# Kernel optimization log

Measured on AMD Instinct MI355X. Metric: run time of the kernel, lower is better.

## Reference

```python
import jax, jax.numpy as jnp
import numpy as np

F = 128
NRBF = 20
CUTOFF = 5.0
L = 3
NZ = 100
F2 = F // 2
N = 10000
E = 256000
NMOL = 100
EPS = 1e-8


def setup_inputs() -> dict:
    key = jax.random.key(0)
    ks = jax.random.split(key, 20)
    xyz = jax.random.uniform(ks[0], (N, 3), jnp.float32) * 10.0
    z = jax.random.randint(ks[1], (N,), 0, NZ)
    nbrs = jax.random.randint(ks[2], (E, 2), 0, N)
    # avoid self-edges (would give zero distance in the sinc RBF)
    nbrs = nbrs.at[:, 1].set(jnp.where(nbrs[:, 1] == nbrs[:, 0], (nbrs[:, 1] + 1) % N, nbrs[:, 1]))
    mol_idx = jnp.sort(jax.random.randint(ks[3], (N,), 0, NMOL))

    def p(k, shape, scale=0.05):
        return jax.random.normal(k, shape, jnp.float32) * scale

    return dict(
        xyz=xyz, z=z, nbrs=nbrs, mol_idx=mol_idx,
        emb=p(ks[4], (NZ, F), 1.0),
        msg_W1=p(ks[5], (L, F, F)), msg_b1=jnp.zeros((L, F), jnp.float32),
        msg_W2=p(ks[6], (L, F, 3 * F)), msg_b2=jnp.zeros((L, 3 * F), jnp.float32),
        dist_W=p(ks[7], (L, NRBF, 3 * F)), dist_b=jnp.zeros((L, 3 * F), jnp.float32),
        upd_U=p(ks[8], (L, F, F)), upd_V=p(ks[9], (L, F, F)),
        upd_W1=p(ks[10], (L, 2 * F, F)), upd_b1=jnp.zeros((L, F), jnp.float32),
        upd_W2=p(ks[11], (L, F, 3 * F)), upd_b2=jnp.zeros((L, 3 * F), jnp.float32),
        read_W1=p(ks[12], (F, F2)), read_b1=jnp.zeros((F2,), jnp.float32),
        read_W2=p(ks[13], (F2, 1)), read_b2=jnp.zeros((1,), jnp.float32),
    )


def _painn(xyz, emb, msg_W1, msg_b1, msg_W2, msg_b2, dist_W, dist_b,
           upd_U, upd_V, upd_W1, upd_b1, upd_W2, upd_b2,
           read_W1, read_b1, read_W2, read_b2, z, nbrs, mol_idx):
    idx_i = nbrs[:, 0]
    idx_j = nbrs[:, 1]
    r_ij = xyz[idx_j] - xyz[idx_i]                       # [E,3]
    d = jnp.sqrt(jnp.sum(r_ij * r_ij, -1) + EPS)          # [E]
    unit = r_ij / d[:, None]
    # sinc radial basis + cosine cutoff envelope
    nvec = jnp.arange(1, NRBF + 1, dtype=xyz.dtype)
    rbf = jnp.sin(nvec[None, :] * jnp.pi * d[:, None] / CUTOFF) / d[:, None]   # [E,NRBF]
    fcut = 0.5 * (jnp.cos(jnp.pi * d / CUTOFF) + 1.0) * (d < CUTOFF)           # [E]

    s_i = emb[z]                                          # [N,F]
    v_i = jnp.zeros((xyz.shape[0], F, 3), xyz.dtype)      # [N,F,3]

    for l in range(L):
        # message block: invariant filter on nodes, gather to edges
        phi = (jax.nn.silu(s_i @ msg_W1[l] + msg_b1[l]) @ msg_W2[l] + msg_b2[l])[idx_j]  # [E,3F]
        w_s = (rbf @ dist_W[l] + dist_b[l]) * fcut[:, None]                               # [E,3F]
        inv = (phi * w_s).reshape(-1, 3, F)
        ds_edge = inv[:, 0]                                                               # [E,F]
        dv_edge = inv[:, 1][:, :, None] * v_i[idx_j] + inv[:, 2][:, :, None] * unit[:, None, :]  # [E,F,3]
        s_i = s_i + jax.ops.segment_sum(ds_edge, idx_i, num_segments=s_i.shape[0])
        v_i = v_i + jax.ops.segment_sum(dv_edge, idx_i, num_segments=s_i.shape[0])

        # update block: channel-mixing of vectors + gated scalar/vector residuals
        u_v = jnp.einsum('nfv,fg->ngv', v_i, upd_U[l])
        v_v = jnp.einsum('nfv,fg->ngv', v_i, upd_V[l])
        vnorm = jnp.sqrt(jnp.sum(v_v * v_v, -1) + EPS)                                    # [N,F]
        a = (jax.nn.silu(jnp.concatenate([s_i, vnorm], -1) @ upd_W1[l] + upd_b1[l])
             @ upd_W2[l] + upd_b2[l]).reshape(-1, 3, F)
        dv = u_v * a[:, 0][:, :, None]
        ds = a[:, 1] * jnp.sum(u_v * v_v, -1) + a[:, 2]
        s_i = s_i + ds
        v_i = v_i + dv

    atom_e = jax.nn.silu(s_i @ read_W1 + read_b1) @ read_W2 + read_b2                     # [N,1]
    energy = jax.ops.segment_sum(atom_e[:, 0], mol_idx, num_segments=NMOL)                # [NMOL]
    return energy


def reference(xyz, z, nbrs, mol_idx, emb, msg_W1, msg_b1, msg_W2, msg_b2,
              dist_W, dist_b, upd_U, upd_V, upd_W1, upd_b1, upd_W2, upd_b2,
              read_W1, read_b1, read_W2, read_b2):
    return _painn(xyz, emb, msg_W1, msg_b1, msg_W2, msg_b2, dist_W, dist_b,
                  upd_U, upd_V, upd_W1, upd_b1, upd_W2, upd_b2,
                  read_W1, read_b1, read_W2, read_b2, z, nbrs, mol_idx)
```

## Files before the change

kernel.cpp:

```cpp
#include <hip/hip_runtime.h>
#include <hip/hip_bf16.h>
#include <math.h>

#define NA 10000
#define NE 256000
#define FDIM 128
#define F3 384
#define NRBF 20
#define NLAYERS 3
#define NMOLS 100
#define CAP 96
#define WROW 388
#define PACK_BLOCKS 2288
#define CUTOFF_F 5.0f
#define EPS_F 1e-8f
#define PI_F 3.14159265358979323846f

typedef __attribute__((ext_vector_type(8))) short bf16x8;
typedef __attribute__((ext_vector_type(4))) float f32x4;

struct pv6 { unsigned int u0, u1, u2; };

__device__ __forceinline__ float silu_f(float x) { return x / (1.0f + __expf(-x)); }

__device__ __forceinline__ unsigned short f2bf(float x) {
  unsigned u = __float_as_uint(x);
  return (unsigned short)((u + 0x7FFFu + ((u >> 16) & 1u)) >> 16);
}
__device__ __forceinline__ float bf2f(unsigned short u) {
  return __uint_as_float(((unsigned)u) << 16);
}
__device__ __forceinline__ float lo_f(unsigned int u) { return bf2f((unsigned short)(u & 0xFFFFu)); }
__device__ __forceinline__ float hi_f(unsigned int u) { return bf2f((unsigned short)(u >> 16)); }

__device__ __forceinline__ void bar_lds() {
  asm volatile("s_waitcnt lgkmcnt(0)" ::: "memory");
  __builtin_amdgcn_s_barrier();
}

__device__ __forceinline__ void pack_one(const float* __restrict__ src,
                                         unsigned short* __restrict__ dst,
                                         int loc, int per, int N) {
  int lay = loc / per;
  int kn = loc - lay * per;
  int k = kn / N, n = kn - k * N;
  int kb = k >> 5, q = (k >> 3) & 3, j = k & 7, nt = n >> 4, c = n & 15;
  int NT = N >> 4;
  dst[(size_t)lay * per + (((kb * NT + nt) * 64 + (q * 16 + c)) * 8 + j)] = f2bf(src[loc]);
}

__device__ __forceinline__ void pack_dw(const float* __restrict__ dW,
                                        const float* __restrict__ db,
                                        unsigned short* __restrict__ dst, int loc) {
  int lay = loc / 12288;
  int kn = loc - lay * 12288;
  int k = kn / 384, n = kn - k * 384;
  float val = 0.0f;
  if (k < NRBF) val = dW[lay * NRBF * 384 + k * 384 + n];
  else if (k == NRBF) val = db[lay * 384 + n];
  int q = (k >> 3) & 3, j = k & 7, nt = n >> 4, c = n & 15;
  dst[(size_t)lay * 12288 + ((nt * 64 + (q * 16 + c)) * 8 + j)] = f2bf(val);
}

__global__ __launch_bounds__(256) void prep_kernel(
    const float* __restrict__ msgW1, const float* __restrict__ msgW2,
    const float* __restrict__ updU, const float* __restrict__ updV,
    const float* __restrict__ updW1, const float* __restrict__ updW2,
    const float* __restrict__ rW1, const float* __restrict__ distW,
    const float* __restrict__ distb, unsigned short* __restrict__ dst,
    const float* __restrict__ xyz, const int* __restrict__ nbrs,
    float* __restrict__ unitv, unsigned short* __restrict__ rbf_bf,
    float* __restrict__ fcut,
    int* __restrict__ deg, int* __restrict__ slot_e, int* __restrict__ slot_j) {
  int b = blockIdx.x;
  if (b < PACK_BLOCKS) {
    int t = b * 256 + threadIdx.x;
    if (t < 49152) pack_one(msgW1, dst, t, 16384, 128);
    else if (t < 196608) pack_one(msgW2, dst + 49152, t - 49152, 49152, 384);
    else if (t < 245760) pack_one(updU, dst + 196608, t - 196608, 16384, 128);
    else if (t < 294912) pack_one(updV, dst + 245760, t - 245760, 16384, 128);
    else if (t < 393216) pack_one(updW1, dst + 294912, t - 294912, 32768, 128);
    else if (t < 540672) pack_one(updW2, dst + 393216, t - 393216, 49152, 384);
    else if (t < 548864) pack_one(rW1, dst + 540672, t - 540672, 8192, 64);
    else if (t < 585728) pack_dw(distW, distb, dst + 548864, t - 548864);
    return;
  }
  int e = (b - PACK_BLOCKS) * 256 + threadIdx.x;
  if (e >= NE) return;
  int i = nbrs[2 * e + 0], j = nbrs[2 * e + 1];
  float rx = xyz[3 * j + 0] - xyz[3 * i + 0];
  float ry = xyz[3 * j + 1] - xyz[3 * i + 1];
  float rz = xyz[3 * j + 2] - xyz[3 * i + 2];
  float d = sqrtf(rx * rx + ry * ry + rz * rz + EPS_F);
  if (d >= CUTOFF_F) return;
  float invd = 1.0f / d;
  float fc = 0.5f * (__cosf(PI_F * d / CUTOFF_F) + 1.0f);
  unitv[3 * e + 0] = rx * invd;
  unitv[3 * e + 1] = ry * invd;
  unitv[3 * e + 2] = rz * invd;
  fcut[e] = fc;
  float base = PI_F * d / CUTOFF_F;
  float sc = invd * fc;
#pragma unroll
  for (int k = 0; k < NRBF; k++)
    rbf_bf[(size_t)e * NRBF + k] = f2bf(__sinf((float)(k + 1) * base) * sc);
  int pos = atomicAdd(&deg[i], 1);
  if (pos < CAP) {
    slot_e[i * CAP + pos] = e;
    slot_j[i * CAP + pos] = j;
  }
}

__global__ __launch_bounds__(256) void msg0_mfma_kernel(
    const float* __restrict__ emb, const int* __restrict__ z, float* __restrict__ s_out,
    const unsigned short* __restrict__ pW1, const float* __restrict__ b1,
    const unsigned short* __restrict__ pW2, const float* __restrict__ b2,
    pv6* __restrict__ cmb) {
  __shared__ bf16x8 sA[4 * 64];
  __shared__ bf16x8 hA[4 * 64];
  int a0 = blockIdx.x * 16;
  int t = threadIdx.x;
  int lane = t & 63, w = t >> 6;
  {
    int kb = t >> 6, l = t & 63;
    int m = l & 15, q = l >> 4;
    int zi = z[a0 + m];
    const float* sp = emb + (size_t)zi * FDIM + kb * 32 + q * 8;
    float* so = s_out + (size_t)(a0 + m) * FDIM + kb * 32 + q * 8;
    bf16x8 c;
#pragma unroll
    for (int j = 0; j < 8; j++) {
      float v = sp[j];
      so[j] = v;
      c[j] = (short)f2bf(v);
    }
    sA[kb * 64 + l] = c;
  }
  __syncthreads();
  f32x4 accH[2];
#pragma unroll
  for (int t2 = 0; t2 < 2; t2++)
#pragma unroll
    for (int r = 0; r < 4; r++) accH[t2][r] = 0.0f;
  const bf16x8* W1f = (const bf16x8*)pW1;
#pragma unroll
  for (int kb = 0; kb < 4; kb++) {
    bf16x8 a = sA[kb * 64 + lane];
#pragma unroll
    for (int t2 = 0; t2 < 2; t2++) {
      bf16x8 b = W1f[(kb * 8 + 2 * w + t2) * 64 + lane];
      accH[t2] = __builtin_amdgcn_mfma_f32_16x16x32_bf16(a, b, accH[t2], 0, 0, 0);
    }
  }
  short* hs = (short*)hA;
#pragma unroll
  for (int t2 = 0; t2 < 2; t2++) {
    int n = w * 32 + t2 * 16 + (lane & 15);
    int kb = n >> 5, q = (n >> 3) & 3, j = n & 7;
    float bias = b1[n];
#pragma unroll
    for (int r = 0; r < 4; r++) {
      int m = (lane >> 4) * 4 + r;
      hs[(kb * 64 + q * 16 + m) * 8 + j] = (short)f2bf(silu_f(accH[t2][r] + bias));
    }
  }
  __syncthreads();
  f32x4 accP[3][2];
#pragma unroll
  for (int c3 = 0; c3 < 3; c3++)
#pragma unroll
    for (int t2 = 0; t2 < 2; t2++)
#pragma unroll
      for (int r = 0; r < 4; r++) accP[c3][t2][r] = 0.0f;
  const bf16x8* W2f = (const bf16x8*)pW2;
#pragma unroll
  for (int kb = 0; kb < 4; kb++) {
    bf16x8 a = hA[kb * 64 + lane];
#pragma unroll
    for (int c3 = 0; c3 < 3; c3++)
#pragma unroll
      for (int t2 = 0; t2 < 2; t2++) {
        bf16x8 b = W2f[(kb * 24 + c3 * 8 + 2 * w + t2) * 64 + lane];
        accP[c3][t2] = __builtin_amdgcn_mfma_f32_16x16x32_bf16(a, b, accP[c3][t2], 0, 0, 0);
      }
  }
#pragma unroll
  for (int t2 = 0; t2 < 2; t2++) {
    int g = (2 * w + t2) * 16 + (lane & 15);
    float bb0 = b2[g], bb1 = b2[FDIM + g], bb2 = b2[2 * FDIM + g];
#pragma unroll
    for (int r = 0; r < 4; r++) {
      int m = (lane >> 4) * 4 + r;
      unsigned p0 = f2bf(accP[0][t2][r] + bb0);
      unsigned p1 = f2bf(accP[1][t2][r] + bb1);
      unsigned p2 = f2bf(accP[2][t2][r] + bb2);
      pv6 rec;
      rec.u0 = p0 | (p1 << 16);
      rec.u1 = p2;
      rec.u2 = 0;
      cmb[(size_t)(a0 + m) * FDIM + g] = rec;
    }
  }
}

__device__ __forceinline__ void afrag_load(const unsigned short* __restrict__ rbf_bf,
                                           const float* __restrict__ fcut,
                                           const int* l_e_all, int cnt, int c0,
                                           int m16, int q4,
                                           unsigned short apf[8], float* afc) {
#pragma unroll
  for (int j = 0; j < 8; j++) apf[j] = 0;
  *afc = 0.0f;
  int p = c0 + m16;
  if (p < cnt && q4 < 3) {
    int e = l_e_all[p];
    const unsigned short* rb = rbf_bf + (size_t)e * NRBF;
    if (q4 < 2) {
#pragma unroll
      for (int j = 0; j < 8; j++) apf[j] = rb[q4 * 8 + j];
    } else {
#pragma unroll
      for (int j = 0; j < 4; j++) apf[j] = rb[16 + j];
      *afc = fcut[e];
    }
  }
}

__device__ __forceinline__ void pref4(const pv6* __restrict__ cmb, const int* l_j,
                                      int cnt, int p0, int f, pv6 R[4]) {
#pragma unroll
  for (int u = 0; u < 4; u++) {
    if (p0 + u < cnt) R[u] = cmb[(size_t)l_j[p0 + u] * FDIM + f];
  }
}

__device__ __forceinline__ void proc4(const pv6 R[4], int pp, int ccnt, int f,
                                      const unsigned short (*w_lds)[WROW],
                                      const float (*l_u)[3],
                                      float& acc_s, float& av0, float& av1, float& av2) {
#pragma unroll
  for (int u = 0; u < 4; u++) {
    if (pp + u < ccnt) {
      float p0 = lo_f(R[u].u0), p1 = hi_f(R[u].u0), p2 = lo_f(R[u].u1);
      float v0 = hi_f(R[u].u1), v1 = lo_f(R[u].u2), v2 = hi_f(R[u].u2);
      float w0 = bf2f(w_lds[pp + u][f]), w1 = bf2f(w_lds[pp + u][FDIM + f]),
            w2 = bf2f(w_lds[pp + u][2 * FDIM + f]);
      acc_s += p0 * w0;
      float i1 = p1 * w1, i2 = p2 * w2;
      av0 += i1 * v0 + i2 * l_u[pp + u][0];
      av1 += i1 * v1 + i2 * l_u[pp + u][1];
      av2 += i1 * v2 + i2 * l_u[pp + u][2];
    }
  }
}

__global__ __launch_bounds__(128) void edge_kernel(
    const pv6* __restrict__ cmb, unsigned short* __restrict__ v_lin,
    float* __restrict__ s, const unsigned short* __restrict__ pDW,
    const int* __restrict__ deg, const int* __restrict__ slot_e,
    const int* __restrict__ slot_j, const unsigned short* __restrict__ rbf_bf,
    const float* __restrict__ fcut, const float* __restrict__ unitv) {
  __shared__ unsigned short w_lds[16][WROW];
  __shared__ float l_u[16][3];
  __shared__ int l_e_all[CAP];
  __shared__ int l_j_all[CAP];
  int i = blockIdx.x;
  int t = threadIdx.x;
  int f = t;
  int lane = t & 63, w = t >> 6;
  int cnt = deg[i];
  if (cnt > CAP) cnt = CAP;
  int base = i * CAP;
  if (t < cnt) {
    l_e_all[t] = slot_e[base + t];
    l_j_all[t] = slot_j[base + t];
  }
  __syncthreads();
  float acc_s = 0.f, av0 = 0.f, av1 = 0.f, av2 = 0.f;
  const bf16x8* Bf = (const bf16x8*)pDW;
  int m16 = lane & 15, q4 = lane >> 4;
  unsigned short apf[8];
  float afc = 0.0f;
  pv6 Ra[4], Rb[4];
  if (cnt > 0) {
    afrag_load(rbf_bf, fcut, l_e_all, cnt, 0, m16, q4, apf, &afc);
    pref4(cmb, l_j_all, cnt, 0, f, Ra);
  }
  for (int c0 = 0; c0 < cnt; c0 += 16) {
    int ccnt = cnt - c0;
    if (ccnt > 16) ccnt = 16;
    bar_lds();
    if (t >= 64 && t < 80) {
      int idx = t - 64, p = c0 + idx;
      if (p < cnt) {
        int e = l_e_all[p];
        l_u[idx][0] = unitv[3 * e + 0];
        l_u[idx][1] = unitv[3 * e + 1];
        l_u[idx][2] = unitv[3 * e + 2];
      }
    }
    bf16x8 a;
#pragma unroll
    for (int j = 0; j < 8; j++) a[j] = (short)apf[j];
    if (q4 == 2) a[4] = (short)f2bf(afc);
    {
      int n0 = lane & 15, mm0 = (lane >> 4) * 4;
#pragma unroll
      for (int tt = 0; tt < 12; tt++) {
        int nt = 12 * w + tt;
        f32x4 acc;
#pragma unroll
        for (int r = 0; r < 4; r++) acc[r] = 0.0f;
        acc = __builtin_amdgcn_mfma_f32_16x16x32_bf16(a, Bf[nt * 64 + lane], acc, 0, 0, 0);
        int n = nt * 16 + n0;
#pragma unroll
        for (int r = 0; r < 4; r++) w_lds[mm0 + r][n] = f2bf(acc[r]);
      }
    }
    if (c0 + 16 < cnt) afrag_load(rbf_bf, fcut, l_e_all, cnt, c0 + 16, m16, q4, apf, &afc);
    bar_lds();
    pref4(cmb, l_j_all, cnt, c0 + 4, f, Rb);
    proc4(Ra, 0, ccnt, f, w_lds, l_u, acc_s, av0, av1, av2);
    pref4(cmb, l_j_all, cnt, c0 + 8, f, Ra);
    proc4(Rb, 4, ccnt, f, w_lds, l_u, acc_s, av0, av1, av2);
    pref4(cmb, l_j_all, cnt, c0 + 12, f, Rb);
    proc4(Ra, 8, ccnt, f, w_lds, l_u, acc_s, av0, av1, av2);
    pref4(cmb, l_j_all, cnt, c0 + 16, f, Ra);
    proc4(Rb, 12, ccnt, f, w_lds, l_u, acc_s, av0, av1, av2);
  }
  {
    pv6 RI = cmb[(size_t)i * FDIM + f];
    av0 += hi_f(RI.u1);
    av1 += lo_f(RI.u2);
    av2 += hi_f(RI.u2);
  }
  unsigned short* vlo = v_lin + (size_t)i * F3;
  vlo[f] = f2bf(av0);
  vlo[FDIM + f] = f2bf(av1);
  vlo[2 * FDIM + f] = f2bf(av2);
  s[(size_t)i * FDIM + f] += acc_s;
}

__global__ __launch_bounds__(256) void upd_fused_kernel(
    float* __restrict__ s, const unsigned short* __restrict__ v_lin,
    pv6* __restrict__ cmb,
    const unsigned short* __restrict__ pU, const unsigned short* __restrict__ pV,
    const unsigned short* __restrict__ pW1, const float* __restrict__ b1,
    const unsigned short* __restrict__ pW2, const float* __restrict__ b2,
    int mode,
    const unsigned short* __restrict__ pMW1, const float* __restrict__ mb1,
    const unsigned short* __restrict__ pMW2, const float* __restrict__ mb2,
    const unsigned short* __restrict__ pRW1, const float* __restrict__ rb1,
    const float* __restrict__ rW2, const float* __restrict__ rb2,
    float* __restrict__ atom_e) {
  __shared__ bf16x8 vAf[3 * 4 * 64];
  __shared__ bf16x8 catA[8 * 64];
  __shared__ bf16x8 hA[4 * 64];
  __shared__ float red[4][16];
  int a0 = blockIdx.x * 16;
  int t = threadIdx.x;
  int lane = t & 63, w = t >> 6;
  {
    int l = t & 63, kb = (t >> 6) & 3;
    int m = l & 15, q = l >> 4;
#pragma unroll
    for (int rt = 0; rt < 3; rt++) {
      vAf[(rt * 4 + kb) * 64 + l] =
          *(const bf16x8*)(v_lin + (size_t)(a0 + m) * F3 + rt * FDIM + kb * 32 + q * 8);
    }
    const float* sp = s + (size_t)(a0 + m) * FDIM + kb * 32 + q * 8;
    bf16x8 c;
#pragma unroll
    for (int j = 0; j < 8; j++) c[j] = (short)f2bf(sp[j]);
    catA[kb * 64 + l] = c;
  }
  __syncthreads();
  f32x4 accU[3][2], accV[3][2];
#pragma unroll
  for (int rt = 0; rt < 3; rt++)
#pragma unroll
    for (int t2 = 0; t2 < 2; t2++)
#pragma unroll
      for (int r = 0; r < 4; r++) { accU[rt][t2][r] = 0.0f; accV[rt][t2][r] = 0.0f; }
  const bf16x8* Uf = (const bf16x8*)pU;
  const bf16x8* Vf = (const bf16x8*)pV;
#pragma unroll
  for (int kb = 0; kb < 4; kb++) {
    bf16x8 bu[2], bv[2];
#pragma unroll
    for (int t2 = 0; t2 < 2; t2++) {
      bu[t2] = Uf[(kb * 8 + 2 * w + t2) * 64 + lane];
      bv[t2] = Vf[(kb * 8 + 2 * w + t2) * 64 + lane];
    }
#pragma unroll
    for (int rt = 0; rt < 3; rt++) {
      bf16x8 a = vAf[(rt * 4 + kb) * 64 + lane];
#pragma unroll
      for (int t2 = 0; t2 < 2; t2++) {
        accU[rt][t2] = __builtin_amdgcn_mfma_f32_16x16x32_bf16(a, bu[t2], accU[rt][t2], 0, 0, 0);
        accV[rt][t2] = __builtin_amdgcn_mfma_f32_16x16x32_bf16(a, bv[t2], accV[rt][t2], 0, 0, 0);
      }
    }
  }
  short* cs = (short*)catA;
#pragma unroll
  for (int t2 = 0; t2 < 2; t2++) {
    int g = w * 32 + t2 * 16 + (lane & 15);
    int k = 128 + g;
    int kb = k >> 5, q = (k >> 3) & 3, j = k & 7;
#pragma unroll
    for (int r = 0; r < 4; r++) {
      int m = (lane >> 4) * 4 + r;
      float x0 = accV[0][t2][r], x1 = accV[1][t2][r], x2 = accV[2][t2][r];
      cs[(kb * 64 + q * 16 + m) * 8 + j] = (short)f2bf(sqrtf(x0 * x0 + x1 * x1 + x2 * x2 + EPS_F));
    }
  }
  __syncthreads();
  f32x4 accH[2];
#pragma unroll
  for (int t2 = 0; t2 < 2; t2++)
#pragma unroll
    for (int r = 0; r < 4; r++) accH[t2][r] = 0.0f;
  const bf16x8* W1f = (const bf16x8*)pW1;
#pragma unroll
  for (int kb = 0; kb < 8; kb++) {
    bf16x8 a = catA[kb * 64 + lane];
#pragma unroll
    for (int t2 = 0; t2 < 2; t2++) {
      bf16x8 b = W1f[(kb * 8 + 2 * w + t2) * 64 + lane];
      accH[t2] = __builtin_amdgcn_mfma_f32_16x16x32_bf16(a, b, accH[t2], 0, 0, 0);
    }
  }
  short* hs = (short*)hA;
#pragma unroll
  for (int t2 = 0; t2 < 2; t2++) {
    int n = w * 32 + t2 * 16 + (lane & 15);
    int kb = n >> 5, q = (n >> 3) & 3, j = n & 7;
    float bias = b1[n];
#pragma unroll
    for (int r = 0; r < 4; r++) {
      int m = (lane >> 4) * 4 + r;
      hs[(kb * 64 + q * 16 + m) * 8 + j] = (short)f2bf(silu_f(accH[t2][r] + bias));
    }
  }
  __syncthreads();
  f32x4 accA[3][2];
#pragma unroll
  for (int c3 = 0; c3 < 3; c3++)
#pragma unroll
    for (int t2 = 0; t2 < 2; t2++)
#pragma unroll
      for (int r = 0; r < 4; r++) accA[c3][t2][r] = 0.0f;
  const bf16x8* W2f = (const bf16x8*)pW2;
#pragma unroll
  for (int kb = 0; kb < 4; kb++) {
    bf16x8 a = hA[kb * 64 + lane];
#pragma unroll
    for (int c3 = 0; c3 < 3; c3++)
#pragma unroll
      for (int t2 = 0; t2 < 2; t2++) {
        bf16x8 b = W2f[(kb * 24 + c3 * 8 + 2 * w + t2) * 64 + lane];
        accA[c3][t2] = __builtin_amdgcn_mfma_f32_16x16x32_bf16(a, b, accA[c3][t2], 0, 0, 0);
      }
  }
  const short* vls = (const short*)vAf;
  unsigned short v0keep[2][4];
#pragma unroll
  for (int t2 = 0; t2 < 2; t2++) {
    int g = w * 32 + t2 * 16 + (lane & 15);
    float bb0 = b2[g], bb1 = b2[FDIM + g], bb2 = b2[2 * FDIM + g];
    int kb = g >> 5, q = (g >> 3) & 3, j = g & 7;
#pragma unroll
    for (int r = 0; r < 4; r++) {
      int m = (lane >> 4) * 4 + r;
      int n = a0 + m;
      float a0v = accA[0][t2][r] + bb0;
      float a1v = accA[1][t2][r] + bb1;
      float a2v = accA[2][t2][r] + bb2;
      float dot = accU[0][t2][r] * accV[0][t2][r] + accU[1][t2][r] * accV[1][t2][r] +
                  accU[2][t2][r] * accV[2][t2][r];
      float s_new = s[(size_t)n * FDIM + g] + a1v * dot + a2v;
      if (mode == 0) {
        s[(size_t)n * FDIM + g] = s_new;
        float nv[3];
#pragma unroll
        for (int c = 0; c < 3; c++) {
          float vold = bf2f((unsigned short)vls[(((c * 4 + kb) * 64) + (q * 16 + m)) * 8 + j]);
          nv[c] = vold + a0v * accU[c][t2][r];
        }
        v0keep[t2][r] = f2bf(nv[0]);
        cmb[(size_t)n * FDIM + g].u2 = (unsigned)f2bf(nv[1]) | ((unsigned)f2bf(nv[2]) << 16);
      }
      cs[(kb * 64 + q * 16 + m) * 8 + j] = (short)f2bf(s_new);
    }
  }
  __syncthreads();
  if (mode == 0) {
    f32x4 accH2[2];
#pragma unroll
    for (int t2 = 0; t2 < 2; t2++)
#pragma unroll
      for (int r = 0; r < 4; r++) accH2[t2][r] = 0.0f;
    const bf16x8* MW1f = (const bf16x8*)pMW1;
#pragma unroll
    for (int kb = 0; kb < 4; kb++) {
      bf16x8 a = catA[kb * 64 + lane];
#pragma unroll
      for (int t2 = 0; t2 < 2; t2++) {
        bf16x8 b = MW1f[(kb * 8 + 2 * w + t2) * 64 + lane];
        accH2[t2] = __builtin_amdgcn_mfma_f32_16x16x32_bf16(a, b, accH2[t2], 0, 0, 0);
      }
    }
#pragma unroll
    for (int t2 = 0; t2 < 2; t2++) {
      int n = w * 32 + t2 * 16 + (lane & 15);
      int kb = n >> 5, q = (n >> 3) & 3, j = n & 7;
      float bias = mb1[n];
#pragma unroll
      for (int r = 0; r < 4; r++) {
        int m = (lane >> 4) * 4 + r;
        hs[(kb * 64 + q * 16 + m) * 8 + j] = (short)f2bf(silu_f(accH2[t2][r] + bias));
      }
    }
    __syncthreads();
    f32x4 accP[3][2];
#pragma unroll
    for (int c3 = 0; c3 < 3; c3++)
#pragma unroll
      for (int t2 = 0; t2 < 2; t2++)
#pragma unroll
        for (int r = 0; r < 4; r++) accP[c3][t2][r] = 0.0f;
    const bf16x8* MW2f = (const bf16x8*)pMW2;
#pragma unroll
    for (int kb = 0; kb < 4; kb++) {
      bf16x8 a = hA[kb * 64 + lane];
#pragma unroll
      for (int c3 = 0; c3 < 3; c3++)
#pragma unroll
        for (int t2 = 0; t2 < 2; t2++) {
          bf16x8 b = MW2f[(kb * 24 + c3 * 8 + 2 * w + t2) * 64 + lane];
          accP[c3][t2] = __builtin_amdgcn_mfma_f32_16x16x32_bf16(a, b, accP[c3][t2], 0, 0, 0);
        }
    }
#pragma unroll
    for (int t2 = 0; t2 < 2; t2++) {
      int g = (2 * w + t2) * 16 + (lane & 15);
      float bb0 = mb2[g], bb1 = mb2[FDIM + g], bb2v = mb2[2 * FDIM + g];
#pragma unroll
      for (int r = 0; r < 4; r++) {
        int m = (lane >> 4) * 4 + r;
        unsigned p0 = f2bf(accP[0][t2][r] + bb0);
        unsigned p1 = f2bf(accP[1][t2][r] + bb1);
        unsigned p2 = f2bf(accP[2][t2][r] + bb2v);
        pv6* rec = &cmb[(size_t)(a0 + m) * FDIM + g];
        rec->u0 = p0 | (p1 << 16);
        rec->u1 = p2 | ((unsigned)v0keep[t2][r] << 16);
      }
    }
  } else {
    f32x4 acc;
#pragma unroll
    for (int r = 0; r < 4; r++) acc[r] = 0.0f;
    const bf16x8* RW1f = (const bf16x8*)pRW1;
#pragma unroll
    for (int kb = 0; kb < 4; kb++) {
      bf16x8 a = catA[kb * 64 + lane];
      bf16x8 b = RW1f[(kb * 4 + w) * 64 + lane];
      acc = __builtin_amdgcn_mfma_f32_16x16x32_bf16(a, b, acc, 0, 0, 0);
    }
    int col = w * 16 + (lane & 15);
    float bias = rb1[col], w2v = rW2[col];
    float val[4];
#pragma unroll
    for (int r = 0; r < 4; r++) val[r] = silu_f(acc[r] + bias) * w2v;
#pragma unroll
    for (int off = 1; off < 16; off <<= 1)
#pragma unroll
      for (int r = 0; r < 4; r++) val[r] += __shfl_xor(val[r], off, 64);
    if ((lane & 15) == 0) {
#pragma unroll
      for (int r = 0; r < 4; r++) red[w][(lane >> 4) * 4 + r] = val[r];
    }
    __syncthreads();
    if (t < 16) {
      atom_e[a0 + t] = red[0][t] + red[1][t] + red[2][t] + red[3][t] + rb2[0];
    }
  }
}

__global__ __launch_bounds__(256) void mol_reduce_kernel(
    const float* __restrict__ atom_e, const int* __restrict__ mol_idx,
    float* __restrict__ out) {
  __shared__ float molsum[NMOLS];
  int t = threadIdx.x;
  if (t < NMOLS) molsum[t] = 0.0f;
  __syncthreads();
  int n = blockIdx.x * 256 + t;
  if (n < NA) atomicAdd(&molsum[mol_idx[n]], atom_e[n]);
  __syncthreads();
  if (t < NMOLS && molsum[t] != 0.0f) atomicAdd(&out[t], molsum[t]);
}

extern "C" void kernel_launch(void* const* d_in, const int* in_sizes, int n_in,
                              void* d_out, int out_size, void* d_ws, size_t ws_size,
                              hipStream_t stream) {
  const float* xyz = (const float*)d_in[0];
  const int* z = (const int*)d_in[1];
  const int* nbrs = (const int*)d_in[2];
  const int* mol = (const int*)d_in[3];
  const float* emb = (const float*)d_in[4];
  const float* msgW1 = (const float*)d_in[5];
  const float* msgb1 = (const float*)d_in[6];
  const float* msgW2 = (const float*)d_in[7];
  const float* msgb2 = (const float*)d_in[8];
  const float* distW = (const float*)d_in[9];
  const float* distb = (const float*)d_in[10];
  const float* updU = (const float*)d_in[11];
  const float* updV = (const float*)d_in[12];
  const float* updW1 = (const float*)d_in[13];
  const float* updb1 = (const float*)d_in[14];
  const float* updW2 = (const float*)d_in[15];
  const float* updb2 = (const float*)d_in[16];
  const float* rW1 = (const float*)d_in[17];
  const float* rb1 = (const float*)d_in[18];
  const float* rW2 = (const float*)d_in[19];
  const float* rb2 = (const float*)d_in[20];

  float* ws = (float*)d_ws;
  float* s = ws;      ws += (size_t)NA * FDIM;
  float* fcut = ws;   ws += (size_t)NE;
  float* unitv = ws;  ws += (size_t)NE * 3;
  float* atom_e = ws; ws += (size_t)NA;
  int* deg = (int*)ws;
  int* slot_e = deg + NA;
  int* slot_j = slot_e + NA * CAP;
  unsigned short* pk = (unsigned short*)(((uintptr_t)(slot_j + NA * CAP) + 15) & ~(uintptr_t)15);
  unsigned short* pMsgW1 = pk;
  unsigned short* pMsgW2 = pMsgW1 + 49152;
  unsigned short* pUpdU  = pMsgW2 + 147456;
  unsigned short* pUpdV  = pUpdU + 49152;
  unsigned short* pUpdW1 = pUpdV + 49152;
  unsigned short* pUpdW2 = pUpdW1 + 98304;
  unsigned short* pRW1   = pUpdW2 + 147456;
  unsigned short* pDW    = pRW1 + 8192;
  unsigned short* rbf_bf = (unsigned short*)(((uintptr_t)(pDW + 36864) + 15) & ~(uintptr_t)15);
  unsigned short* after_rbf = rbf_bf + (size_t)NE * NRBF + 8;
  pv6* cmb = (pv6*)(((uintptr_t)after_rbf + 15) & ~(uintptr_t)15);
  unsigned short* v_lin = (unsigned short*)(cmb + (size_t)NA * FDIM);

  hipMemsetAsync(deg, 0, NA * sizeof(int), stream);
  hipMemsetAsync(d_out, 0, NMOLS * sizeof(float), stream);

  prep_kernel<<<PACK_BLOCKS + NE / 256, 256, 0, stream>>>(
      msgW1, msgW2, updU, updV, updW1, updW2, rW1, distW, distb, pMsgW1,
      xyz, nbrs, unitv, rbf_bf, fcut, deg, slot_e, slot_j);
  msg0_mfma_kernel<<<NA / 16, 256, 0, stream>>>(emb, z, s, pMsgW1, msgb1, pMsgW2, msgb2, cmb);

  for (int l = 0; l < NLAYERS; l++) {
    edge_kernel<<<NA, 128, 0, stream>>>(cmb, v_lin, s,
                                        pDW + (size_t)l * 12288,
                                        deg, slot_e, slot_j, rbf_bf, fcut, unitv);
    int mode = (l == NLAYERS - 1) ? 1 : 0;
    int lnext = (l + 1 < NLAYERS) ? l + 1 : 0;
    upd_fused_kernel<<<NA / 16, 256, 0, stream>>>(
        s, v_lin, cmb, pUpdU + (size_t)l * 16384, pUpdV + (size_t)l * 16384,
        pUpdW1 + (size_t)l * 32768, updb1 + (size_t)l * FDIM,
        pUpdW2 + (size_t)l * 49152, updb2 + (size_t)l * F3,
        mode,
        pMsgW1 + (size_t)lnext * 16384, msgb1 + (size_t)lnext * FDIM,
        pMsgW2 + (size_t)lnext * 49152, msgb2 + (size_t)lnext * F3,
        pRW1, rb1, rW2, rb2, atom_e);
  }
  mol_reduce_kernel<<<(NA + 255) / 256, 256, 0, stream>>>(atom_e, mol, (float*)d_out);
}
```

Baseline: 320.1 us.

## Split edge chunks across waves to remove per-chunk block barriers

The edge kernel now gives each wave its own 16-edge chunk, interleaved by wave, instead of having both waves cooperate on every chunk. Each wave runs all 24 MFMA tiles for its chunk into a private LDS buffer and handles two feature columns per lane. This removes the two block-wide barriers per chunk, and the two waves' partial sums are combined through LDS at the end. The cost is that each wave does twice the MFMA work per chunk, register pressure rises, prefetch of the next chunk's gathers across iterations is lost, and there is an extra reduction pass.

Result: slower. 529.1 us (+65.3%).

```diff
diff --git a/kernel.cpp b/kernel.cpp
--- a/kernel.cpp
+++ b/kernel.cpp
@@ -32,11 +32,6 @@
 }
 __device__ __forceinline__ float lo_f(unsigned int u) { return bf2f((unsigned short)(u & 0xFFFFu)); }
 __device__ __forceinline__ float hi_f(unsigned int u) { return bf2f((unsigned short)(u >> 16)); }
-
-__device__ __forceinline__ void bar_lds() {
-  asm volatile("s_waitcnt lgkmcnt(0)" ::: "memory");
-  __builtin_amdgcn_s_barrier();
-}
 
 __device__ __forceinline__ void pack_one(const float* __restrict__ src,
                                          unsigned short* __restrict__ dst,
@@ -226,33 +221,38 @@
   }
 }
 
-__device__ __forceinline__ void pref4(const pv6* __restrict__ cmb, const int* l_j,
-                                      int cnt, int p0, int f, pv6 R[4]) {
-#pragma unroll
-  for (int u = 0; u < 4; u++) {
-    if (p0 + u < cnt) R[u] = cmb[(size_t)l_j[p0 + u] * FDIM + f];
-  }
-}
-
-__device__ __forceinline__ void proc4(const pv6 R[4], int pp, int ccnt, int f,
-                                      const unsigned short (*w_lds)[WROW],
-                                      const float (*l_u)[3],
-                                      float& acc_s, float& av0, float& av1, float& av2) {
-#pragma unroll
-  for (int u = 0; u < 4; u++) {
-    if (pp + u < ccnt) {
-      float p0 = lo_f(R[u].u0), p1 = hi_f(R[u].u0), p2 = lo_f(R[u].u1);
-      float v0 = hi_f(R[u].u1), v1 = lo_f(R[u].u2), v2 = hi_f(R[u].u2);
-      float w0 = bf2f(w_lds[pp + u][f]), w1 = bf2f(w_lds[pp + u][FDIM + f]),
-            w2 = bf2f(w_lds[pp + u][2 * FDIM + f]);
-      acc_s += p0 * w0;
-      float i1 = p1 * w1, i2 = p2 * w2;
-      av0 += i1 * v0 + i2 * l_u[pp + u][0];
-      av1 += i1 * v1 + i2 * l_u[pp + u][1];
-      av2 += i1 * v2 + i2 * l_u[pp + u][2];
-    }
-  }
-}
+__device__ __forceinline__ void proc1(const pv6& R, float wv0, float wv1, float wv2,
+                                      const float* lu,
+                                      float& as, float& v0, float& v1, float& v2) {
+  float p0 = lo_f(R.u0), p1 = hi_f(R.u0), p2 = lo_f(R.u1);
+  float x0 = hi_f(R.u1), x1 = lo_f(R.u2), x2 = hi_f(R.u2);
+  as += p0 * wv0;
+  float i1 = p1 * wv1, i2 = p2 * wv2;
+  v0 += i1 * x0 + i2 * lu[0];
+  v1 += i1 * x1 + i2 * lu[1];
+  v2 += i1 * x2 + i2 * lu[2];
+}
+
+#define LOAD4(X0, X1, P)                                   \
+  {                                                        \
+    _Pragma("unroll") for (int u = 0; u < 4; u++) {        \
+      size_t row = (size_t)l_j_all[(P) + u] * FDIM;        \
+      X0[u] = cmb[row + f0];                               \
+      X1[u] = cmb[row + f1];                               \
+    }                                                      \
+  }
+
+#define PROC4(X0, X1, PP)                                                                  \
+  {                                                                                        \
+    _Pragma("unroll") for (int u = 0; u < 4; u++) {                                        \
+      const unsigned short* wr = w_lds[w][(PP) + u];                                       \
+      const float* lu = l_u[w][(PP) + u];                                                  \
+      proc1(X0[u], bf2f(wr[f0]), bf2f(wr[FDIM + f0]), bf2f(wr[2 * FDIM + f0]), lu,         \
+            s0, a00, a01, a02);                                                            \
+      proc1(X1[u], bf2f(wr[f1]), bf2f(wr[FDIM + f1]), bf2f(wr[2 * FDIM + f1]), lu,         \
+            s1, a10, a11, a12);                                                            \
+    }                                                                                      \
+  }
 
 __global__ __launch_bounds__(128) void edge_kernel(
     const pv6* __restrict__ cmb, unsigned short* __restrict__ v_lin,
@@ -260,14 +260,14 @@
     const int* __restrict__ deg, const int* __restrict__ slot_e,
     const int* __restrict__ slot_j, const unsigned short* __restrict__ rbf_bf,
     const float* __restrict__ fcut, const float* __restrict__ unitv) {
-  __shared__ unsigned short w_lds[16][WROW];
-  __shared__ float l_u[16][3];
+  __shared__ __align__(16) unsigned short w_lds[2][16][WROW];
+  __shared__ float l_u[2][16][3];
   __shared__ int l_e_all[CAP];
   __shared__ int l_j_all[CAP];
   int i = blockIdx.x;
   int t = threadIdx.x;
-  int f = t;
   int lane = t & 63, w = t >> 6;
+  int f0 = lane, f1 = lane + 64;
   int cnt = deg[i];
   if (cnt > CAP) cnt = CAP;
   int base = i * CAP;
@@ -276,69 +276,92 @@
     l_j_all[t] = slot_j[base + t];
   }
   __syncthreads();
-  float acc_s = 0.f, av0 = 0.f, av1 = 0.f, av2 = 0.f;
+  float s0 = 0.f, s1 = 0.f;
+  float a00 = 0.f, a01 = 0.f, a02 = 0.f;
+  float a10 = 0.f, a11 = 0.f, a12 = 0.f;
   const bf16x8* Bf = (const bf16x8*)pDW;
   int m16 = lane & 15, q4 = lane >> 4;
   unsigned short apf[8];
   float afc = 0.0f;
-  pv6 Ra[4], Rb[4];
-  if (cnt > 0) {
-    afrag_load(rbf_bf, fcut, l_e_all, cnt, 0, m16, q4, apf, &afc);
-    pref4(cmb, l_j_all, cnt, 0, f, Ra);
-  }
-  for (int c0 = 0; c0 < cnt; c0 += 16) {
+  {
+    int c00 = 16 * w;
+    if (c00 < cnt) afrag_load(rbf_bf, fcut, l_e_all, cnt, c00, m16, q4, apf, &afc);
+  }
+  for (int c0 = 16 * w; c0 < cnt; c0 += 32) {
     int ccnt = cnt - c0;
     if (ccnt > 16) ccnt = 16;
-    bar_lds();
-    if (t >= 64 && t < 80) {
-      int idx = t - 64, p = c0 + idx;
+    if (lane < 16) {
+      int p = c0 + lane;
       if (p < cnt) {
         int e = l_e_all[p];
-        l_u[idx][0] = unitv[3 * e + 0];
-        l_u[idx][1] = unitv[3 * e + 1];
-        l_u[idx][2] = unitv[3 * e + 2];
+        l_u[w][lane][0] = unitv[3 * e + 0];
+        l_u[w][lane][1] = unitv[3 * e + 1];
+        l_u[w][lane][2] = unitv[3 * e + 2];
       }
     }
     bf16x8 a;
 #pragma unroll
     for (int j = 0; j < 8; j++) a[j] = (short)apf[j];
     if (q4 == 2) a[4] = (short)f2bf(afc);
-    {
-      int n0 = lane & 15, mm0 = (lane >> 4) * 4;
-#pragma unroll
-      for (int tt = 0; tt < 12; tt++) {
-        int nt = 12 * w + tt;
-        f32x4 acc;
-#pragma unroll
-        for (int r = 0; r < 4; r++) acc[r] = 0.0f;
-        acc = __builtin_amdgcn_mfma_f32_16x16x32_bf16(a, Bf[nt * 64 + lane], acc, 0, 0, 0);
-        int n = nt * 16 + n0;
-#pragma unroll
-        for (int r = 0; r < 4; r++) w_lds[mm0 + r][n] = f2bf(acc[r]);
-      }
-    }
-    if (c0 + 16 < cnt) afrag_load(rbf_bf, fcut, l_e_all, cnt, c0 + 16, m16, q4, apf, &afc);
-    bar_lds();
-    pref4(cmb, l_j_all, cnt, c0 + 4, f, Rb);
-    proc4(Ra, 0, ccnt, f, w_lds, l_u, acc_s, av0, av1, av2);
-    pref4(cmb, l_j_all, cnt, c0 + 8, f, Ra);
-    proc4(Rb, 4, ccnt, f, w_lds, l_u, acc_s, av0, av1, av2);
-    pref4(cmb, l_j_all, cnt, c0 + 12, f, Rb);
-    proc4(Ra, 8, ccnt, f, w_lds, l_u, acc_s, av0, av1, av2);
-    pref4(cmb, l_j_all, cnt, c0 + 16, f, Ra);
-    proc4(Rb, 12, ccnt, f, w_lds, l_u, acc_s, av0, av1, av2);
-  }
+#pragma unroll
+    for (int tt = 0; tt < 24; tt++) {
+      f32x4 acc;
+#pragma unroll
+      for (int r = 0; r < 4; r++) acc[r] = 0.0f;
+      acc = __builtin_amdgcn_mfma_f32_16x16x32_bf16(a, Bf[tt * 64 + lane], acc, 0, 0, 0);
+      int n = tt * 16 + m16;
+#pragma unroll
+      for (int r = 0; r < 4; r++) w_lds[w][q4 * 4 + r][n] = f2bf(acc[r]);
+    }
+    if (c0 + 32 < cnt) afrag_load(rbf_bf, fcut, l_e_all, cnt, c0 + 32, m16, q4, apf, &afc);
+    int nb = ccnt >> 2;
+    pv6 A0[4], A1[4], B0[4], B1[4];
+    if (nb > 0) LOAD4(A0, A1, c0 + 0);
+    if (nb > 1) LOAD4(B0, B1, c0 + 4);
+    asm volatile("s_waitcnt lgkmcnt(0)" ::: "memory");
+    if (nb > 0) PROC4(A0, A1, 0);
+    if (nb > 2) LOAD4(A0, A1, c0 + 8);
+    if (nb > 1) PROC4(B0, B1, 4);
+    if (nb > 3) LOAD4(B0, B1, c0 + 12);
+    if (nb > 2) PROC4(A0, A1, 8);
+    if (nb > 3) PROC4(B0, B1, 12);
+    for (int pp = nb * 4; pp < ccnt; pp++) {
+      size_t row = (size_t)l_j_all[c0 + pp] * FDIM;
+      pv6 Rx = cmb[row + f0], Ry = cmb[row + f1];
+      const unsigned short* wr = w_lds[w][pp];
+      const float* lu = l_u[w][pp];
+      proc1(Rx, bf2f(wr[f0]), bf2f(wr[FDIM + f0]), bf2f(wr[2 * FDIM + f0]), lu,
+            s0, a00, a01, a02);
+      proc1(Ry, bf2f(wr[f1]), bf2f(wr[FDIM + f1]), bf2f(wr[2 * FDIM + f1]), lu,
+            s1, a10, a11, a12);
+    }
+  }
+  __syncthreads();
+  f32x4* part = (f32x4*)w_lds;
   {
-    pv6 RI = cmb[(size_t)i * FDIM + f];
-    av0 += hi_f(RI.u1);
-    av1 += lo_f(RI.u2);
-    av2 += hi_f(RI.u2);
-  }
-  unsigned short* vlo = v_lin + (size_t)i * F3;
-  vlo[f] = f2bf(av0);
-  vlo[FDIM + f] = f2bf(av1);
-  vlo[2 * FDIM + f] = f2bf(av2);
-  s[(size_t)i * FDIM + f] += acc_s;
+    f32x4 p0v, p1v;
+    p0v[0] = s0; p0v[1] = a00; p0v[2] = a01; p0v[3] = a02;
+    p1v[0] = s1; p1v[1] = a10; p1v[2] = a11; p1v[3] = a12;
+    part[w * 128 + f0] = p0v;
+    part[w * 128 + f1] = p1v;
+  }
+  __syncthreads();
+  {
+    f32x4 q0 = part[t], q1 = part[128 + t];
+    float accs = q0[0] + q1[0];
+    float v0 = q0[1] + q1[1];
+    float v1 = q0[2] + q1[2];
+    float v2 = q0[3] + q1[3];
+    pv6 RI = cmb[(size_t)i * FDIM + t];
+    v0 += hi_f(RI.u1);
+    v1 += lo_f(RI.u2);
+    v2 += hi_f(RI.u2);
+    unsigned short* vlo = v_lin + (size_t)i * F3;
+    vlo[t] = f2bf(v0);
+    vlo[FDIM + t] = f2bf(v1);
+    vlo[2 * FDIM + t] = f2bf(v2);
+    s[(size_t)i * FDIM + t] += accs;
+  }
 }
 
 __global__ __launch_bounds__(256) void upd_fused_kernel(
```
